# Optimization experiments

Hardware: AMD Instinct MI355X
Metric: run time of the kernel (lower is better)

The kernel has to match this reference:

```python
import jax, jax.numpy as jnp
import numpy as np

TEMPERATURE = 0.02


def setup_inputs() -> dict:
    key = jax.random.key(0)
    kq, kp = jax.random.split(key)
    query_embeddings = jax.random.normal(kq, (32, 32, 128), dtype=jnp.float32)      # [b, s, h]
    positive_embeddings = jax.random.normal(kp, (512, 128, 128), dtype=jnp.float32)  # [c, d, h]
    return {"query_embeddings": query_embeddings, "positive_embeddings": positive_embeddings}


def reference(query_embeddings, positive_embeddings):
    # Late interaction: all query tokens vs all doc tokens across the (in-)batch.
    # [b, c, s, d]
    late = jnp.einsum('bsh,cdh->bcsd', query_embeddings, positive_embeddings)
    # MaxSim: max over doc tokens, sum over query tokens -> [b, c]
    scores = late.max(axis=-1).sum(axis=-1) / TEMPERATURE
    # CrossEntropyLoss(reduction='mean') with labels = zeros(b)
    loss = jnp.mean(jax.nn.logsumexp(scores, axis=-1) - scores[:, 0])
    return loss
```

## Files before the change

kernel.cpp:

```cpp
#include <hip/hip_runtime.h>

#define BQ 32
#define H  128
#define C  512
#define D  128

typedef _Float16 half8v __attribute__((ext_vector_type(8)));
typedef float floatx4 __attribute__((ext_vector_type(4)));

__global__ __launch_bounds__(256) void qprep_kernel(const float* __restrict__ q,
                                                    _Float16* __restrict__ qs,
                                                    float* __restrict__ out) {
  int t = blockIdx.x * 256 + threadIdx.x;
  if (t == 0) out[0] = 0.0f;
  int lane = t & 63;
  int st   = (t >> 6) & 1;
  int kb   = (t >> 7) & 3;
  int b    = t >> 9;
  int s    = st * 16 + (lane & 15);
  int h    = kb * 32 + (lane >> 4) * 8;
  const float* src = q + ((b * 32 + s) * H + h);
  float4 v0 = *(const float4*)src;
  float4 v1 = *(const float4*)(src + 4);
  half8v o = { (_Float16)v0.x, (_Float16)v0.y, (_Float16)v0.z, (_Float16)v0.w,
               (_Float16)v1.x, (_Float16)v1.y, (_Float16)v1.z, (_Float16)v1.w };
  *(half8v*)(qs + (size_t)t * 8) = o;
}

__global__ __launch_bounds__(256, 2) void scores_kernel(const float* __restrict__ pos,
                                                        const _Float16* __restrict__ qs,
                                                        float* __restrict__ scores) {
  const int c    = blockIdx.x;
  const int tid  = threadIdx.x;
  const int w    = tid >> 6;
  const int lane = tid & 63;
  const int quad = lane >> 4;
  const int mrow = lane & 15;

  __shared__ float pmm[BQ][4][32];

  const half8v* qf = (const half8v*)qs;
  const float*  pc = pos + (size_t)c * (D * H);

  half8v  pa[2][4];
  half8v  qb[2][2][4];
  floatx4 acc[2][2][2];

#pragma unroll
  for (int nt = 0; nt < 2; ++nt)
#pragma unroll
    for (int kb = 0; kb < 4; ++kb) {
      qb[0][nt][kb] = qf[(kb * 2 + nt) * 64 + lane];
      qb[1][nt][kb] = qf[(( (1 * 4) + kb) * 2 + nt) * 64 + lane];
    }

#pragma unroll
  for (int kb = 0; kb < 4; ++kb)
#pragma unroll
    for (int mt2 = 0; mt2 < 2; ++mt2) {
      const float* src = pc + ((w * 32 + mt2 * 16 + mrow) * H + kb * 32 + quad * 8);
      float4 v0 = *(const float4*)src;
      float4 v1 = *(const float4*)(src + 4);
      half8v f = { (_Float16)v0.x, (_Float16)v0.y, (_Float16)v0.z, (_Float16)v0.w,
                   (_Float16)v1.x, (_Float16)v1.y, (_Float16)v1.z, (_Float16)v1.w };
      pa[mt2][kb] = f;
    }

  auto reduce_store = [&](int b, floatx4 (&a)[2][2]) {
    float t0 = fmaxf(fmaxf(fmaxf(a[0][0][0], a[0][0][1]), fmaxf(a[0][0][2], a[0][0][3])),
                     fmaxf(fmaxf(a[1][0][0], a[1][0][1]), fmaxf(a[1][0][2], a[1][0][3])));
    float t1 = fmaxf(fmaxf(fmaxf(a[0][1][0], a[0][1][1]), fmaxf(a[0][1][2], a[0][1][3])),
                     fmaxf(fmaxf(a[1][1][0], a[1][1][1]), fmaxf(a[1][1][2], a[1][1][3])));
    t0 = fmaxf(t0, __shfl_xor(t0, 16));
    t0 = fmaxf(t0, __shfl_xor(t0, 32));
    t1 = fmaxf(t1, __shfl_xor(t1, 16));
    t1 = fmaxf(t1, __shfl_xor(t1, 32));
    float v = (lane < 16) ? t0 : t1;
    if (lane < 32) pmm[b][w][lane] = v;
  };

#pragma unroll
  for (int mt2 = 0; mt2 < 2; ++mt2)
#pragma unroll
    for (int nt = 0; nt < 2; ++nt) { floatx4 z = {0.f, 0.f, 0.f, 0.f}; acc[0][mt2][nt] = z; }
#pragma unroll
  for (int kb = 0; kb < 4; ++kb)
#pragma unroll
    for (int mt2 = 0; mt2 < 2; ++mt2)
#pragma unroll
      for (int nt = 0; nt < 2; ++nt)
        acc[0][mt2][nt] = __builtin_amdgcn_mfma_f32_16x16x32_f16(
            pa[mt2][kb], qb[0][nt][kb], acc[0][mt2][nt], 0, 0, 0);

#pragma unroll
  for (int b = 1; b < BQ; ++b) {
    const int cur = b & 1, prv = cur ^ 1;
    if (b + 1 < BQ) {
#pragma unroll
      for (int nt = 0; nt < 2; ++nt)
#pragma unroll
        for (int kb = 0; kb < 4; ++kb)
          qb[prv][nt][kb] = qf[(((b + 1) * 4 + kb) * 2 + nt) * 64 + lane];
    }
#pragma unroll
    for (int mt2 = 0; mt2 < 2; ++mt2)
#pragma unroll
      for (int nt = 0; nt < 2; ++nt) { floatx4 z = {0.f, 0.f, 0.f, 0.f}; acc[cur][mt2][nt] = z; }
#pragma unroll
    for (int kb = 0; kb < 4; ++kb)
#pragma unroll
      for (int mt2 = 0; mt2 < 2; ++mt2)
#pragma unroll
        for (int nt = 0; nt < 2; ++nt)
          acc[cur][mt2][nt] = __builtin_amdgcn_mfma_f32_16x16x32_f16(
              pa[mt2][kb], qb[cur][nt][kb], acc[cur][mt2][nt], 0, 0, 0);
    reduce_store(b - 1, acc[prv]);
  }
  reduce_store(BQ - 1, acc[1]);

  __syncthreads();

  {
    int b  = tid >> 3;
    int sq = tid & 7;
    float4 x0 = *(float4*)&pmm[b][0][sq * 4];
    float4 x1 = *(float4*)&pmm[b][1][sq * 4];
    float4 x2 = *(float4*)&pmm[b][2][sq * 4];
    float4 x3 = *(float4*)&pmm[b][3][sq * 4];
    float mx_x = fmaxf(fmaxf(x0.x, x1.x), fmaxf(x2.x, x3.x));
    float mx_y = fmaxf(fmaxf(x0.y, x1.y), fmaxf(x2.y, x3.y));
    float mx_z = fmaxf(fmaxf(x0.z, x1.z), fmaxf(x2.z, x3.z));
    float mx_w = fmaxf(fmaxf(x0.w, x1.w), fmaxf(x2.w, x3.w));
    float v = (mx_x + mx_y) + (mx_z + mx_w);
    v += __shfl_xor(v, 1);
    v += __shfl_xor(v, 2);
    v += __shfl_xor(v, 4);
    if (sq == 0) scores[b * C + c] = v * 50.0f;
  }
}

__global__ __launch_bounds__(256) void loss_kernel(const float* __restrict__ scores,
                                                   float* __restrict__ out) {
  __shared__ float red[8];
  const int b = blockIdx.x, tid = threadIdx.x, w = tid >> 6, lane = tid & 63;
  const float* row = scores + b * C;
  float x0 = row[tid], x1 = row[tid + 256];
  float mx = fmaxf(x0, x1);
#pragma unroll
  for (int off = 1; off < 64; off <<= 1) mx = fmaxf(mx, __shfl_xor(mx, off));
  if (lane == 0) red[w] = mx;
  __syncthreads();
  float bmax = fmaxf(fmaxf(red[0], red[1]), fmaxf(red[2], red[3]));
  float e = __expf(x0 - bmax) + __expf(x1 - bmax);
#pragma unroll
  for (int off = 1; off < 64; off <<= 1) e += __shfl_xor(e, off);
  if (lane == 0) red[4 + w] = e;
  __syncthreads();
  if (tid == 0) {
    float s = red[4] + red[5] + red[6] + red[7];
    atomicAdd(out, (bmax + __logf(s) - row[0]) * (1.0f / 32.0f));
  }
}

extern "C" void kernel_launch(void* const* d_in, const int* in_sizes, int n_in,
                              void* d_out, int out_size, void* d_ws, size_t ws_size,
                              hipStream_t stream) {
  const float* q = (const float*)d_in[0];
  const float* p = (const float*)d_in[1];
  float* scores  = (float*)d_ws;
  _Float16* qs   = (_Float16*)((char*)d_ws + 65536);

  qprep_kernel<<<64, 256, 0, stream>>>(q, qs, (float*)d_out);
  scores_kernel<<<C, 256, 0, stream>>>(p, qs, scores);
  loss_kernel<<<32, 256, 0, stream>>>(scores, (float*)d_out);
}
```

Baseline: 96.47 us.

## Switch MaxSim GEMM to 32x32x16 MFMA with triple-buffered query fragments

Replaces the 2x2 grid of 16x16x32 f16 MFMAs per wave with a single 32x32x16 MFMA chain over eight k-steps. The query pre-pack layout changes to match the new operand layout, and query fragments are now held in three rotating buffers instead of two. The row-max reduction over the accumulator needs only one cross-lane shuffle instead of four. The aim is fewer instructions and less shuffle overhead per batch. The trade-off is a longer dependent MFMA chain per accumulator, which may hurt latency hiding.

```diff
diff --git a/kernel.cpp b/kernel.cpp
--- a/kernel.cpp
+++ b/kernel.cpp
@@ -6,7 +6,7 @@
 #define D  128
 
 typedef _Float16 half8v __attribute__((ext_vector_type(8)));
-typedef float floatx4 __attribute__((ext_vector_type(4)));
+typedef float floatx16 __attribute__((ext_vector_type(16)));
 
 __global__ __launch_bounds__(256) void qprep_kernel(const float* __restrict__ q,
                                                     _Float16* __restrict__ qs,
@@ -14,11 +14,10 @@
   int t = blockIdx.x * 256 + threadIdx.x;
   if (t == 0) out[0] = 0.0f;
   int lane = t & 63;
-  int st   = (t >> 6) & 1;
-  int kb   = (t >> 7) & 3;
+  int kb   = (t >> 6) & 7;
   int b    = t >> 9;
-  int s    = st * 16 + (lane & 15);
-  int h    = kb * 32 + (lane >> 4) * 8;
+  int s    = lane & 31;
+  int h    = kb * 16 + (lane >> 5) * 8;
   const float* src = q + ((b * 32 + s) * H + h);
   float4 v0 = *(const float4*)src;
   float4 v1 = *(const float4*)(src + 4);
@@ -34,86 +33,66 @@
   const int tid  = threadIdx.x;
   const int w    = tid >> 6;
   const int lane = tid & 63;
-  const int quad = lane >> 4;
-  const int mrow = lane & 15;
+  const int mrow = lane & 31;
+  const int khi  = (lane >> 5) * 8;
 
   __shared__ float pmm[BQ][4][32];
 
   const half8v* qf = (const half8v*)qs;
   const float*  pc = pos + (size_t)c * (D * H);
 
-  half8v  pa[2][4];
-  half8v  qb[2][2][4];
-  floatx4 acc[2][2][2];
+  half8v   pa[8];
+  half8v   qb[3][8];
+  floatx16 acc[2];
+
+  floatx16 zc;
+#pragma unroll
+  for (int i = 0; i < 16; ++i) zc[i] = 0.0f;
 
 #pragma unroll
-  for (int nt = 0; nt < 2; ++nt)
-#pragma unroll
-    for (int kb = 0; kb < 4; ++kb) {
-      qb[0][nt][kb] = qf[(kb * 2 + nt) * 64 + lane];
-      qb[1][nt][kb] = qf[(( (1 * 4) + kb) * 2 + nt) * 64 + lane];
-    }
+  for (int kb = 0; kb < 8; ++kb) {
+    const float* src = pc + ((w * 32 + mrow) * H + kb * 16 + khi);
+    float4 v0 = *(const float4*)src;
+    float4 v1 = *(const float4*)(src + 4);
+    half8v f = { (_Float16)v0.x, (_Float16)v0.y, (_Float16)v0.z, (_Float16)v0.w,
+                 (_Float16)v1.x, (_Float16)v1.y, (_Float16)v1.z, (_Float16)v1.w };
+    pa[kb] = f;
+  }
 
 #pragma unroll
-  for (int kb = 0; kb < 4; ++kb)
+  for (int kb = 0; kb < 8; ++kb) qb[0][kb] = qf[kb * 64 + lane];
 #pragma unroll
-    for (int mt2 = 0; mt2 < 2; ++mt2) {
-      const float* src = pc + ((w * 32 + mt2 * 16 + mrow) * H + kb * 32 + quad * 8);
-      float4 v0 = *(const float4*)src;
-      float4 v1 = *(const float4*)(src + 4);
-      half8v f = { (_Float16)v0.x, (_Float16)v0.y, (_Float16)v0.z, (_Float16)v0.w,
-                   (_Float16)v1.x, (_Float16)v1.y, (_Float16)v1.z, (_Float16)v1.w };
-      pa[mt2][kb] = f;
-    }
+  for (int kb = 0; kb < 8; ++kb) qb[1][kb] = qf[(8 + kb) * 64 + lane];
 
-  auto reduce_store = [&](int b, floatx4 (&a)[2][2]) {
-    float t0 = fmaxf(fmaxf(fmaxf(a[0][0][0], a[0][0][1]), fmaxf(a[0][0][2], a[0][0][3])),
-                     fmaxf(fmaxf(a[1][0][0], a[1][0][1]), fmaxf(a[1][0][2], a[1][0][3])));
-    float t1 = fmaxf(fmaxf(fmaxf(a[0][1][0], a[0][1][1]), fmaxf(a[0][1][2], a[0][1][3])),
-                     fmaxf(fmaxf(a[1][1][0], a[1][1][1]), fmaxf(a[1][1][2], a[1][1][3])));
-    t0 = fmaxf(t0, __shfl_xor(t0, 16));
-    t0 = fmaxf(t0, __shfl_xor(t0, 32));
-    t1 = fmaxf(t1, __shfl_xor(t1, 16));
-    t1 = fmaxf(t1, __shfl_xor(t1, 32));
-    float v = (lane < 16) ? t0 : t1;
-    if (lane < 32) pmm[b][w][lane] = v;
+  auto reduce_store = [&](int b, floatx16& a) {
+    float m01 = fmaxf(fmaxf(a[0],  a[1]),  fmaxf(a[2],  a[3]));
+    float m23 = fmaxf(fmaxf(a[4],  a[5]),  fmaxf(a[6],  a[7]));
+    float m45 = fmaxf(fmaxf(a[8],  a[9]),  fmaxf(a[10], a[11]));
+    float m67 = fmaxf(fmaxf(a[12], a[13]), fmaxf(a[14], a[15]));
+    float m = fmaxf(fmaxf(m01, m23), fmaxf(m45, m67));
+    m = fmaxf(m, __shfl_xor(m, 32));
+    if (lane < 32) pmm[b][w][lane] = m;
   };
 
+  acc[0] = __builtin_amdgcn_mfma_f32_32x32x16_f16(pa[0], qb[0][0], zc, 0, 0, 0);
 #pragma unroll
-  for (int mt2 = 0; mt2 < 2; ++mt2)
-#pragma unroll
-    for (int nt = 0; nt < 2; ++nt) { floatx4 z = {0.f, 0.f, 0.f, 0.f}; acc[0][mt2][nt] = z; }
-#pragma unroll
-  for (int kb = 0; kb < 4; ++kb)
-#pragma unroll
-    for (int mt2 = 0; mt2 < 2; ++mt2)
-#pragma unroll
-      for (int nt = 0; nt < 2; ++nt)
-        acc[0][mt2][nt] = __builtin_amdgcn_mfma_f32_16x16x32_f16(
-            pa[mt2][kb], qb[0][nt][kb], acc[0][mt2][nt], 0, 0, 0);
+  for (int kb = 1; kb < 8; ++kb)
+    acc[0] = __builtin_amdgcn_mfma_f32_32x32x16_f16(pa[kb], qb[0][kb], acc[0], 0, 0, 0);
 
 #pragma unroll
   for (int b = 1; b < BQ; ++b) {
     const int cur = b & 1, prv = cur ^ 1;
     if (b + 1 < BQ) {
+      const int nb = (b + 1) * 8;
+      half8v* dst = qb[(b + 1) % 3];
 #pragma unroll
-      for (int nt = 0; nt < 2; ++nt)
+      for (int kb = 0; kb < 8; ++kb) dst[kb] = qf[(nb + kb) * 64 + lane];
+    }
+    const half8v* qc = qb[b % 3];
+    acc[cur] = __builtin_amdgcn_mfma_f32_32x32x16_f16(pa[0], qc[0], zc, 0, 0, 0);
 #pragma unroll
-        for (int kb = 0; kb < 4; ++kb)
-          qb[prv][nt][kb] = qf[(((b + 1) * 4 + kb) * 2 + nt) * 64 + lane];
-    }
-#pragma unroll
-    for (int mt2 = 0; mt2 < 2; ++mt2)
-#pragma unroll
-      for (int nt = 0; nt < 2; ++nt) { floatx4 z = {0.f, 0.f, 0.f, 0.f}; acc[cur][mt2][nt] = z; }
-#pragma unroll
-    for (int kb = 0; kb < 4; ++kb)
-#pragma unroll
-      for (int mt2 = 0; mt2 < 2; ++mt2)
-#pragma unroll
-        for (int nt = 0; nt < 2; ++nt)
-          acc[cur][mt2][nt] = __builtin_amdgcn_mfma_f32_16x16x32_f16(
-              pa[mt2][kb], qb[cur][nt][kb], acc[cur][mt2][nt], 0, 0, 0);
+    for (int kb = 1; kb < 8; ++kb)
+      acc[cur] = __builtin_amdgcn_mfma_f32_32x32x16_f16(pa[kb], qc[kb], acc[cur], 0, 0, 0);
     reduce_store(b - 1, acc[prv]);
   }
   reduce_store(BQ - 1, acc[1]);
```

New measurement: 96.42 us. No clear change (-0.0%).
